# Optimization experiments

Hardware: AMD Instinct MI355X
Metric: run time of the kernel (lower is better)

The kernel has to match this reference:

```python
import jax, jax.numpy as jnp
import numpy as np

B, N, S, C1, C2, CIN, CO = 16, 4096, 1024, 128, 256, 384, 128
BN_EPS = 1e-5


def _bn(x, g, b):
    # BatchNorm1d in training mode: biased batch stats over (B, L) per channel.
    m = x.mean(axis=(0, 1))
    v = x.var(axis=(0, 1))
    return (x - m) * jax.lax.rsqrt(v + BN_EPS) * g + b


def _gelu(x):
    return jax.nn.gelu(x, approximate=False)  # torch nn.GELU default (erf)


def _conv1x1(x, w, b):
    # x: (B, L, Cin), w: (Cout, Cin) -> (B, L, Cout)
    return jnp.einsum('blc,oc->blo', x, w) + b


def setup_inputs() -> dict:
    ks = jax.random.split(jax.random.key(0), 20)
    sc = 0.05
    return {
        'xyz1': jax.random.normal(ks[0], (B, N, 3), jnp.float32),
        'xyz2': jax.random.normal(ks[1], (B, S, 3), jnp.float32),
        'points1': jax.random.normal(ks[2], (B, N, C1), jnp.float32),
        'points2': jax.random.normal(ks[3], (B, S, C2), jnp.float32),
        'fuse_w': jax.random.normal(ks[4], (CO, CIN), jnp.float32) * sc,
        'fuse_b': jax.random.normal(ks[5], (CO,), jnp.float32) * sc,
        'fuse_g': jnp.ones((CO,), jnp.float32),
        'fuse_bt': jnp.zeros((CO,), jnp.float32),
        'w1': jax.random.normal(ks[6], (CO, CO), jnp.float32) * sc,
        'b1': jax.random.normal(ks[7], (CO,), jnp.float32) * sc,
        'g1': jnp.ones((CO,), jnp.float32),
        'bt1': jnp.zeros((CO,), jnp.float32),
        'w2': jax.random.normal(ks[8], (CO, CO), jnp.float32) * sc,
        'b2': jax.random.normal(ks[9], (CO,), jnp.float32) * sc,
        'g2': jnp.ones((CO,), jnp.float32),
        'bt2': jnp.zeros((CO,), jnp.float32),
    }


def reference(xyz1, xyz2, points1, points2,
              fuse_w, fuse_b, fuse_g, fuse_bt,
              w1, b1, g1, bt1, w2, b2, g2, bt2):
    # pairwise euclidean distances (B, N, S) without (B,N,S,3) intermediate
    sq = (jnp.sum(xyz1 * xyz1, -1)[:, :, None]
          + jnp.sum(xyz2 * xyz2, -1)[:, None, :]
          - 2.0 * jnp.einsum('bnd,bsd->bns', xyz1, xyz2))
    dists = jnp.sqrt(jnp.maximum(sq, 1e-12))
    # 3 nearest neighbors, ascending distance
    neg_d3, idx = jax.lax.top_k(-dists, 3)        # (B, N, 3)
    d3 = -neg_d3
    dist_recip = 1.0 / (d3 + 1e-8)
    weight = dist_recip / jnp.sum(dist_recip, axis=-1, keepdims=True)
    gathered = points2[jnp.arange(B)[:, None, None], idx]  # (B, N, 3, C2)
    interp = jnp.sum(gathered * weight[..., None], axis=2)  # (B, N, C2)

    new_points = jnp.concatenate([points1, interp], axis=-1)  # (B, N, CIN)
    x = _gelu(_bn(_conv1x1(new_points, fuse_w, fuse_b), fuse_g, fuse_bt))
    # ConvBNReLURes1D block (groups=1, res_expansion=1.0)
    h = _gelu(_bn(_conv1x1(x, w1, b1), g1, bt1))
    h = _bn(_conv1x1(h, w2, b2), g2, bt2)
    return _gelu(h + x)  # (B, N, CO)
```

## Files before the change

### kernel.cpp

```cpp
#include <hip/hip_runtime.h>
#include <hip/hip_bf16.h>
#include <math.h>

#define B_   16
#define N_   4096
#define S_   1024
#define C1_  128
#define C2_  256
#define CIN_ 384
#define CO_  128
#define ROWS (B_ * N_)

typedef __attribute__((ext_vector_type(8))) __bf16 bf16x8;
typedef __attribute__((ext_vector_type(8))) short  s16x8;
typedef __attribute__((ext_vector_type(4))) float  f32x4;

__device__ inline float bf2f(short s) {
  unsigned u = ((unsigned)(unsigned short)s) << 16;
  float f; __builtin_memcpy(&f, &u, 4); return f;
}
__device__ inline short f2bf(float f) {
  __hip_bfloat16 h = __float2bfloat16(f);
  short s; __builtin_memcpy(&s, &h, 2); return s;
}
__device__ inline float gelu_f(float v) {
  return 0.5f * v * (1.f + erff(v * 0.70710678118654752f));
}
__device__ inline f32x4 mfma_bf16(s16x8 a, s16x8 b, f32x4 c) {
  return __builtin_amdgcn_mfma_f32_16x16x32_bf16(
      __builtin_bit_cast(bf16x8, a), __builtin_bit_cast(bf16x8, b), c, 0, 0, 0);
}

__global__ __launch_bounds__(256) void prep_kernel(
    const float* __restrict__ fw, const float* __restrict__ w1,
    const float* __restrict__ w2, short* __restrict__ fwb,
    short* __restrict__ w1b, short* __restrict__ w2b, float* __restrict__ stats)
{
  int i = blockIdx.x * 256 + threadIdx.x;
  if (i < CO_ * CIN_) fwb[i] = f2bf(fw[i]);
  if (i < CO_ * CO_) { w1b[i] = f2bf(w1[i]); w2b[i] = f2bf(w2[i]); }
  if (i < 768) stats[i] = 0.f;
}

__global__ __launch_bounds__(256) void knn_kernel(
    const float* __restrict__ xyz1, const float* __restrict__ xyz2,
    int* __restrict__ idxs, float* __restrict__ wts)
{
  __shared__ float4 pts[S_];
  const int b = blockIdx.y;
  const float* p2 = xyz2 + (size_t)b * S_ * 3;
  for (int j = threadIdx.x; j < S_; j += 256) {
    float x = p2[j*3+0], y = p2[j*3+1], z = p2[j*3+2];
    pts[j] = make_float4(x, y, z, x*x + y*y + z*z);
  }
  __syncthreads();
  const int n = blockIdx.x * 256 + threadIdx.x;
  const float* q = xyz1 + ((size_t)b * N_ + n) * 3;
  const float qx = q[0], qy = q[1], qz = q[2];
  const float qq = qx*qx + qy*qy + qz*qz;
  float d0 = 3.4e38f, d1 = 3.4e38f, d2 = 3.4e38f;
  int   i0 = 0, i1 = 0, i2 = 0;
  #pragma unroll 4
  for (int j = 0; j < S_; ++j) {
    float4 p = pts[j];
    float d = qq + p.w - 2.f * (qx*p.x + qy*p.y + qz*p.z);
    bool c2 = d < d2;
    d2 = c2 ? d : d2;  i2 = c2 ? j : i2;
    bool c1 = d2 < d1;
    float td = d1; int ti = i1;
    d1 = c1 ? d2 : d1; i1 = c1 ? i2 : i1;
    d2 = c1 ? td : d2; i2 = c1 ? ti : i2;
    bool c0 = d1 < d0;
    td = d0; ti = i0;
    d0 = c0 ? d1 : d0; i0 = c0 ? i1 : i0;
    d1 = c0 ? td : d1; i1 = c0 ? ti : i1;
  }
  float r0 = 1.f / (sqrtf(fmaxf(d0, 1e-12f)) + 1e-8f);
  float r1 = 1.f / (sqrtf(fmaxf(d1, 1e-12f)) + 1e-8f);
  float r2 = 1.f / (sqrtf(fmaxf(d2, 1e-12f)) + 1e-8f);
  float rs = 1.f / (r0 + r1 + r2);
  size_t o = ((size_t)b * N_ + n) * 3;
  idxs[o+0] = i0; idxs[o+1] = i1; idxs[o+2] = i2;
  wts [o+0] = r0*rs; wts[o+1] = r1*rs; wts[o+2] = r2*rs;
}

__global__ __launch_bounds__(384) void interp_kernel(
    const float* __restrict__ points1, const float* __restrict__ points2,
    const int* __restrict__ idxs, const float* __restrict__ wts,
    short* __restrict__ np_out)
{
  const int rid = blockIdx.x;
  const int b = rid >> 12;
  const int t = threadIdx.x;
  short* out = np_out + (size_t)rid * CIN_;
  if (t < C1_) {
    out[t] = f2bf(points1[(size_t)rid * C1_ + t]);
  } else {
    const int c = t - C1_;
    const int* id = idxs + (size_t)rid * 3;
    const float* w = wts + (size_t)rid * 3;
    const float* p2 = points2 + (size_t)b * S_ * C2_;
    float v = w[0] * p2[(size_t)id[0] * C2_ + c]
            + w[1] * p2[(size_t)id[1] * C2_ + c]
            + w[2] * p2[(size_t)id[2] * C2_ + c];
    out[t] = f2bf(v);
  }
}

template<int K>
__global__ __launch_bounds__(256) void gemm_bn_kernel(
    const short* __restrict__ A, const short* __restrict__ W,
    short* __restrict__ Raw, float* __restrict__ gsum, float* __restrict__ gsq)
{
  const int tid  = threadIdx.x;
  const int wave = tid >> 6, lane = tid & 63;
  const int l16  = lane & 15, lk = lane >> 4;
  const int row0 = blockIdx.x * 128 + wave * 32;

  __shared__ float ssum[CO_], ssq[CO_];
  if (tid < CO_) { ssum[tid] = 0.f; ssq[tid] = 0.f; }

  f32x4 acc[2][8];
  #pragma unroll
  for (int m = 0; m < 2; ++m)
    #pragma unroll
    for (int n = 0; n < 8; ++n) acc[m][n] = f32x4{0.f, 0.f, 0.f, 0.f};

  const short* a0 = A + (size_t)(row0 + l16) * K + lk * 8;
  const short* a1 = a0 + (size_t)16 * K;
  const short* w0 = W + (size_t)l16 * K + lk * 8;

  #pragma unroll 4
  for (int kk = 0; kk < K; kk += 32) {
    s16x8 af0 = *(const s16x8*)(a0 + kk);
    s16x8 af1 = *(const s16x8*)(a1 + kk);
    s16x8 wf[8];
    #pragma unroll
    for (int n = 0; n < 8; ++n)
      wf[n] = *(const s16x8*)(w0 + (size_t)n * 16 * K + kk);
    #pragma unroll
    for (int n = 0; n < 8; ++n) {
      acc[0][n] = mfma_bf16(af0, wf[n], acc[0][n]);
      acc[1][n] = mfma_bf16(af1, wf[n], acc[1][n]);
    }
  }
  __syncthreads();

  #pragma unroll
  for (int n = 0; n < 8; ++n) {
    float s = 0.f, q = 0.f;
    #pragma unroll
    for (int m = 0; m < 2; ++m)
      #pragma unroll
      for (int r = 0; r < 4; ++r) { float v = acc[m][n][r]; s += v; q += v*v; }
    s += __shfl_xor(s, 16); q += __shfl_xor(q, 16);
    s += __shfl_xor(s, 32); q += __shfl_xor(q, 32);
    if (lane < 16) {
      atomicAdd(&ssum[n*16 + l16], s);
      atomicAdd(&ssq [n*16 + l16], q);
    }
  }

  #pragma unroll
  for (int m = 0; m < 2; ++m)
    #pragma unroll
    for (int n = 0; n < 8; ++n)
      #pragma unroll
      for (int r = 0; r < 4; ++r) {
        int row = row0 + m*16 + lk*4 + r;
        Raw[(size_t)row * CO_ + n*16 + l16] = f2bf(acc[m][n][r]);
      }

  __syncthreads();
  if (tid < CO_)      atomicAdd(&gsum[tid],        ssum[tid]);
  else                atomicAdd(&gsq [tid - CO_],  ssq [tid - CO_]);
}

template<bool FINAL>
__global__ __launch_bounds__(256) void bn_act_kernel(
    const short* __restrict__ raw, const float* __restrict__ gsum,
    const float* __restrict__ gsq, const float* __restrict__ gamma,
    const float* __restrict__ beta, const short* __restrict__ xres,
    void* __restrict__ outp)
{
  __shared__ float ssc[CO_], ssh[CO_];
  const int tid = threadIdx.x;
  if (tid < CO_) {
    const float inv = 1.f / (float)ROWS;
    float mean = gsum[tid] * inv;
    float var  = gsq[tid] * inv - mean * mean;
    float sc   = gamma[tid] * rsqrtf(var + 1e-5f);
    ssc[tid] = sc;
    ssh[tid] = beta[tid] - mean * sc;
  }
  __syncthreads();
  const int gid = blockIdx.x * 256 + tid;
  float sc[8], sh[8];
  const int cpos = (gid & 15) * 8;
  #pragma unroll
  for (int j = 0; j < 8; ++j) { sc[j] = ssc[cpos + j]; sh[j] = ssh[cpos + j]; }
  const int NCHUNK = ROWS * CO_ / 8;
  const int stride = gridDim.x * 256;
  for (int ch = gid; ch < NCHUNK; ch += stride) {
    s16x8 rv = ((const s16x8*)raw)[ch];
    if (!FINAL) {
      s16x8 ov;
      #pragma unroll
      for (int j = 0; j < 8; ++j)
        ov[j] = f2bf(gelu_f(bf2f(rv[j]) * sc[j] + sh[j]));
      ((s16x8*)outp)[ch] = ov;
    } else {
      s16x8 xv = ((const s16x8*)xres)[ch];
      f32x4 o0, o1;
      #pragma unroll
      for (int j = 0; j < 4; ++j)
        o0[j] = gelu_f(bf2f(rv[j]) * sc[j] + sh[j] + bf2f(xv[j]));
      #pragma unroll
      for (int j = 0; j < 4; ++j)
        o1[j] = gelu_f(bf2f(rv[j+4]) * sc[j+4] + sh[j+4] + bf2f(xv[j+4]));
      ((f32x4*)outp)[2*(size_t)ch]     = o0;
      ((f32x4*)outp)[2*(size_t)ch + 1] = o1;
    }
  }
}

extern "C" void kernel_launch(void* const* d_in, const int* in_sizes, int n_in,
                              void* d_out, int out_size, void* d_ws, size_t ws_size,
                              hipStream_t stream) {
  const float* xyz1    = (const float*)d_in[0];
  const float* xyz2    = (const float*)d_in[1];
  const float* points1 = (const float*)d_in[2];
  const float* points2 = (const float*)d_in[3];
  const float* fuse_w  = (const float*)d_in[4];
  const float* fuse_g  = (const float*)d_in[6];
  const float* fuse_bt = (const float*)d_in[7];
  const float* w1      = (const float*)d_in[8];
  const float* g1      = (const float*)d_in[10];
  const float* bt1     = (const float*)d_in[11];
  const float* w2      = (const float*)d_in[12];
  const float* g2      = (const float*)d_in[14];
  const float* bt2     = (const float*)d_in[15];

  char* ws = (char*)d_ws;
  short* np_b  = (short*)(ws);
  short* x_b   = (short*)(ws);
  short* h_b   = (short*)(ws + 16777216);
  short* raw   = (short*)(ws + 50331648);
  short* wf_b  = (short*)(ws + 67108864);
  short* w1_b  = (short*)(ws + 67207168);
  short* w2_b  = (short*)(ws + 67239936);
  int*   idxs  = (int*)  (ws + 67272704);
  float* wts   = (float*)(ws + 68059136);
  float* stats = (float*)(ws + 68845568);
  float *sum1 = stats,       *sq1 = stats + 128;
  float *sum2 = stats + 256, *sq2 = stats + 384;
  float *sum3 = stats + 512, *sq3 = stats + 640;

  prep_kernel<<<192, 256, 0, stream>>>(fuse_w, w1, w2, wf_b, w1_b, w2_b, stats);
  knn_kernel<<<dim3(N_/256, B_), 256, 0, stream>>>(xyz1, xyz2, idxs, wts);
  interp_kernel<<<ROWS, 384, 0, stream>>>(points1, points2, idxs, wts, np_b);

  gemm_bn_kernel<CIN_><<<ROWS/128, 256, 0, stream>>>(np_b, wf_b, raw, sum1, sq1);
  bn_act_kernel<false><<<2048, 256, 0, stream>>>(raw, sum1, sq1, fuse_g, fuse_bt, nullptr, x_b);

  gemm_bn_kernel<CO_><<<ROWS/128, 256, 0, stream>>>(x_b, w1_b, raw, sum2, sq2);
  bn_act_kernel<false><<<2048, 256, 0, stream>>>(raw, sum2, sq2, g1, bt1, nullptr, h_b);

  gemm_bn_kernel<CO_><<<ROWS/128, 256, 0, stream>>>(h_b, w2_b, raw, sum3, sq3);
  bn_act_kernel<true><<<2048, 256, 0, stream>>>(raw, sum3, sq3, g2, bt2, x_b, d_out);
}
```

Before: 358.6 us.

## Fuse interpolation into first GEMM, split KNN across 8 lanes per query

Removes the separate interp kernel and its bf16 intermediate by gathering and weighting points2 rows and converting points1 directly inside the first GEMM's K loop. The KNN kernel now assigns 8 threads per query, each scanning a strided subset of candidates, then merges partial top-3 lists with xor shuffles; it also drops qq from the inner loop and adds it back at the end. The GEMM is transposed so weights are the A operand, and the epilogue writes 4-wide bf16 vectors with a shuffle-based stats reduction. The fused GEMM now performs scattered fp32 gathers inside its inner loop, which may stall the MFMA pipeline.

```diff
diff --git a/kernel.cpp b/kernel.cpp
--- a/kernel.cpp
+++ b/kernel.cpp
@@ -13,6 +13,7 @@
 
 typedef __attribute__((ext_vector_type(8))) __bf16 bf16x8;
 typedef __attribute__((ext_vector_type(8))) short  s16x8;
+typedef __attribute__((ext_vector_type(4))) short  s16x4;
 typedef __attribute__((ext_vector_type(4))) float  f32x4;
 
 __device__ inline float bf2f(short s) {
@@ -29,6 +30,12 @@
 __device__ inline f32x4 mfma_bf16(s16x8 a, s16x8 b, f32x4 c) {
   return __builtin_amdgcn_mfma_f32_16x16x32_bf16(
       __builtin_bit_cast(bf16x8, a), __builtin_bit_cast(bf16x8, b), c, 0, 0, 0);
+}
+__device__ inline s16x8 pack8(f32x4 a, f32x4 b) {
+  s16x8 r;
+  #pragma unroll
+  for (int j = 0; j < 4; ++j) { r[j] = f2bf(a[j]); r[j+4] = f2bf(b[j]); }
+  return r;
 }
 
 __global__ __launch_bounds__(256) void prep_kernel(
@@ -48,63 +55,154 @@
 {
   __shared__ float4 pts[S_];
   const int b = blockIdx.y;
-  const float* p2 = xyz2 + (size_t)b * S_ * 3;
+  const float* pp = xyz2 + (size_t)b * S_ * 3;
   for (int j = threadIdx.x; j < S_; j += 256) {
-    float x = p2[j*3+0], y = p2[j*3+1], z = p2[j*3+2];
+    float x = pp[j*3+0], y = pp[j*3+1], z = pp[j*3+2];
     pts[j] = make_float4(x, y, z, x*x + y*y + z*z);
   }
   __syncthreads();
-  const int n = blockIdx.x * 256 + threadIdx.x;
+  const int t   = blockIdx.x * 256 + threadIdx.x;
+  const int n   = t >> 3;
+  const int sub = t & 7;
   const float* q = xyz1 + ((size_t)b * N_ + n) * 3;
   const float qx = q[0], qy = q[1], qz = q[2];
   const float qq = qx*qx + qy*qy + qz*qz;
+
   float d0 = 3.4e38f, d1 = 3.4e38f, d2 = 3.4e38f;
   int   i0 = 0, i1 = 0, i2 = 0;
-  #pragma unroll 4
-  for (int j = 0; j < S_; ++j) {
-    float4 p = pts[j];
-    float d = qq + p.w - 2.f * (qx*p.x + qy*p.y + qz*p.z);
-    bool c2 = d < d2;
-    d2 = c2 ? d : d2;  i2 = c2 ? j : i2;
-    bool c1 = d2 < d1;
-    float td = d1; int ti = i1;
+  auto ins = [&](float d, int i) {
+    bool c2 = d < d2;  d2 = c2 ? d : d2;  i2 = c2 ? i : i2;
+    bool c1 = d2 < d1; float td = d1; int ti = i1;
     d1 = c1 ? d2 : d1; i1 = c1 ? i2 : i1;
     d2 = c1 ? td : d2; i2 = c1 ? ti : i2;
-    bool c0 = d1 < d0;
-    td = d0; ti = i0;
+    bool c0 = d1 < d0; td = d0; ti = i0;
     d0 = c0 ? d1 : d0; i0 = c0 ? i1 : i0;
     d1 = c0 ? td : d1; i1 = c0 ? ti : i1;
-  }
-  float r0 = 1.f / (sqrtf(fmaxf(d0, 1e-12f)) + 1e-8f);
-  float r1 = 1.f / (sqrtf(fmaxf(d1, 1e-12f)) + 1e-8f);
-  float r2 = 1.f / (sqrtf(fmaxf(d2, 1e-12f)) + 1e-8f);
-  float rs = 1.f / (r0 + r1 + r2);
-  size_t o = ((size_t)b * N_ + n) * 3;
-  idxs[o+0] = i0; idxs[o+1] = i1; idxs[o+2] = i2;
-  wts [o+0] = r0*rs; wts[o+1] = r1*rs; wts[o+2] = r2*rs;
-}
-
-__global__ __launch_bounds__(384) void interp_kernel(
-    const float* __restrict__ points1, const float* __restrict__ points2,
+  };
+  #pragma unroll 4
+  for (int it = 0; it < S_ / 8; ++it) {
+    int j = it * 8 + sub;
+    float4 p = pts[j];
+    float dot = fmaf(qz, p.z, fmaf(qy, p.y, qx * p.x));
+    float d = fmaf(-2.f, dot, p.w);
+    ins(d, j);
+  }
+  #pragma unroll
+  for (int delta = 1; delta < 8; delta <<= 1) {
+    float e0 = __shfl_xor(d0, delta), e1 = __shfl_xor(d1, delta), e2 = __shfl_xor(d2, delta);
+    int   j0 = __shfl_xor(i0, delta), j1 = __shfl_xor(i1, delta), j2 = __shfl_xor(i2, delta);
+    ins(e0, j0); ins(e1, j1); ins(e2, j2);
+  }
+  if (sub == 0) {
+    float r0 = 1.f / (sqrtf(fmaxf(d0 + qq, 1e-12f)) + 1e-8f);
+    float r1 = 1.f / (sqrtf(fmaxf(d1 + qq, 1e-12f)) + 1e-8f);
+    float r2 = 1.f / (sqrtf(fmaxf(d2 + qq, 1e-12f)) + 1e-8f);
+    float rs = 1.f / (r0 + r1 + r2);
+    size_t o = ((size_t)b * N_ + n) * 3;
+    idxs[o+0] = i0; idxs[o+1] = i1; idxs[o+2] = i2;
+    wts [o+0] = r0*rs; wts[o+1] = r1*rs; wts[o+2] = r2*rs;
+  }
+}
+
+__device__ inline void epilogue_store_stats(
+    f32x4 (&acc)[8][2], int row0, int l16, int lk,
+    short* __restrict__ Raw, float* __restrict__ ssum, float* __restrict__ ssq)
+{
+  #pragma unroll
+  for (int m = 0; m < 8; ++m) {
+    f32x4 sv = acc[m][0] + acc[m][1];
+    f32x4 qv = acc[m][0]*acc[m][0] + acc[m][1]*acc[m][1];
+    #pragma unroll
+    for (int r = 0; r < 4; ++r) {
+      float s = sv[r], q = qv[r];
+      s += __shfl_xor(s, 1); q += __shfl_xor(q, 1);
+      s += __shfl_xor(s, 2); q += __shfl_xor(q, 2);
+      s += __shfl_xor(s, 4); q += __shfl_xor(q, 4);
+      s += __shfl_xor(s, 8); q += __shfl_xor(q, 8);
+      if (l16 == 0) {
+        int c = m*16 + lk*4 + r;
+        atomicAdd(&ssum[c], s); atomicAdd(&ssq[c], q);
+      }
+    }
+    #pragma unroll
+    for (int nf = 0; nf < 2; ++nf) {
+      s16x4 pv;
+      #pragma unroll
+      for (int r = 0; r < 4; ++r) pv[r] = f2bf(acc[m][nf][r]);
+      *(s16x4*)(Raw + (size_t)(row0 + nf*16 + l16) * CO_ + m*16 + lk*4) = pv;
+    }
+  }
+}
+
+__global__ __launch_bounds__(256) void gemm1_fused_kernel(
+    const float* __restrict__ p1, const float* __restrict__ p2,
     const int* __restrict__ idxs, const float* __restrict__ wts,
-    short* __restrict__ np_out)
-{
-  const int rid = blockIdx.x;
-  const int b = rid >> 12;
-  const int t = threadIdx.x;
-  short* out = np_out + (size_t)rid * CIN_;
-  if (t < C1_) {
-    out[t] = f2bf(points1[(size_t)rid * C1_ + t]);
-  } else {
-    const int c = t - C1_;
-    const int* id = idxs + (size_t)rid * 3;
-    const float* w = wts + (size_t)rid * 3;
-    const float* p2 = points2 + (size_t)b * S_ * C2_;
-    float v = w[0] * p2[(size_t)id[0] * C2_ + c]
-            + w[1] * p2[(size_t)id[1] * C2_ + c]
-            + w[2] * p2[(size_t)id[2] * C2_ + c];
-    out[t] = f2bf(v);
-  }
+    const short* __restrict__ W, short* __restrict__ Raw,
+    float* __restrict__ gsum, float* __restrict__ gsq)
+{
+  const int tid  = threadIdx.x;
+  const int wave = tid >> 6, lane = tid & 63;
+  const int l16  = lane & 15, lk = lane >> 4;
+  const int row0 = blockIdx.x * 128 + wave * 32;
+
+  __shared__ float ssum[CO_], ssq[CO_];
+  if (tid < CO_) { ssum[tid] = 0.f; ssq[tid] = 0.f; }
+
+  const int r0 = row0 + l16, r1 = r0 + 16;
+  const int bb = row0 >> 12;
+  const float* p2b = p2 + (size_t)bb * S_ * C2_;
+  const float* ga0 = p2b + (size_t)idxs[(size_t)r0*3+0] * C2_;
+  const float* ga1 = p2b + (size_t)idxs[(size_t)r0*3+1] * C2_;
+  const float* ga2 = p2b + (size_t)idxs[(size_t)r0*3+2] * C2_;
+  const float  wa0 = wts[(size_t)r0*3+0], wa1 = wts[(size_t)r0*3+1], wa2 = wts[(size_t)r0*3+2];
+  const float* gb0 = p2b + (size_t)idxs[(size_t)r1*3+0] * C2_;
+  const float* gb1 = p2b + (size_t)idxs[(size_t)r1*3+1] * C2_;
+  const float* gb2 = p2b + (size_t)idxs[(size_t)r1*3+2] * C2_;
+  const float  wb0 = wts[(size_t)r1*3+0], wb1 = wts[(size_t)r1*3+1], wb2 = wts[(size_t)r1*3+2];
+
+  f32x4 acc[8][2];
+  #pragma unroll
+  for (int m = 0; m < 8; ++m)
+    #pragma unroll
+    for (int nf = 0; nf < 2; ++nf) acc[m][nf] = f32x4{0.f,0.f,0.f,0.f};
+
+  const short* wbase = W + (size_t)l16 * CIN_ + lk * 8;
+  const float* p1r0  = p1 + (size_t)r0 * C1_ + lk * 8;
+  const float* p1r1  = p1 + (size_t)r1 * C1_ + lk * 8;
+
+  #pragma unroll
+  for (int kk = 0; kk < 128; kk += 32) {
+    s16x8 bf0 = pack8(*(const f32x4*)(p1r0 + kk), *(const f32x4*)(p1r0 + kk + 4));
+    s16x8 bf1 = pack8(*(const f32x4*)(p1r1 + kk), *(const f32x4*)(p1r1 + kk + 4));
+    #pragma unroll
+    for (int m = 0; m < 8; ++m) {
+      s16x8 wf = *(const s16x8*)(wbase + (size_t)m*16*CIN_ + kk);
+      acc[m][0] = mfma_bf16(wf, bf0, acc[m][0]);
+      acc[m][1] = mfma_bf16(wf, bf1, acc[m][1]);
+    }
+  }
+  #pragma unroll 4
+  for (int kk2 = 0; kk2 < 256; kk2 += 32) {
+    const int c = kk2 + lk * 8;
+    f32x4 v0a = wa0 * *(const f32x4*)(ga0 + c)     + wa1 * *(const f32x4*)(ga1 + c)     + wa2 * *(const f32x4*)(ga2 + c);
+    f32x4 v0b = wa0 * *(const f32x4*)(ga0 + c + 4) + wa1 * *(const f32x4*)(ga1 + c + 4) + wa2 * *(const f32x4*)(ga2 + c + 4);
+    f32x4 v1a = wb0 * *(const f32x4*)(gb0 + c)     + wb1 * *(const f32x4*)(gb1 + c)     + wb2 * *(const f32x4*)(gb2 + c);
+    f32x4 v1b = wb0 * *(const f32x4*)(gb0 + c + 4) + wb1 * *(const f32x4*)(gb1 + c + 4) + wb2 * *(const f32x4*)(gb2 + c + 4);
+    s16x8 bf0 = pack8(v0a, v0b);
+    s16x8 bf1 = pack8(v1a, v1b);
+    #pragma unroll
+    for (int m = 0; m < 8; ++m) {
+      s16x8 wf = *(const s16x8*)(wbase + (size_t)m*16*CIN_ + 128 + kk2);
+      acc[m][0] = mfma_bf16(wf, bf0, acc[m][0]);
+      acc[m][1] = mfma_bf16(wf, bf1, acc[m][1]);
+    }
+  }
+
+  __syncthreads();
+  epilogue_store_stats(acc, row0, l16, lk, Raw, ssum, ssq);
+  __syncthreads();
+  if (tid < CO_)      atomicAdd(&gsum[tid],       ssum[tid]);
+  else                atomicAdd(&gsq[tid - CO_],  ssq[tid - CO_]);
 }
 
 template<int K>
@@ -120,60 +218,33 @@
   __shared__ float ssum[CO_], ssq[CO_];
   if (tid < CO_) { ssum[tid] = 0.f; ssq[tid] = 0.f; }
 
-  f32x4 acc[2][8];
-  #pragma unroll
-  for (int m = 0; m < 2; ++m)
-    #pragma unroll
-    for (int n = 0; n < 8; ++n) acc[m][n] = f32x4{0.f, 0.f, 0.f, 0.f};
-
-  const short* a0 = A + (size_t)(row0 + l16) * K + lk * 8;
-  const short* a1 = a0 + (size_t)16 * K;
-  const short* w0 = W + (size_t)l16 * K + lk * 8;
+  f32x4 acc[8][2];
+  #pragma unroll
+  for (int m = 0; m < 8; ++m)
+    #pragma unroll
+    for (int nf = 0; nf < 2; ++nf) acc[m][nf] = f32x4{0.f,0.f,0.f,0.f};
+
+  const short* a0    = A + (size_t)(row0 + l16) * K + lk * 8;
+  const short* a1    = a0 + (size_t)16 * K;
+  const short* wbase = W + (size_t)l16 * K + lk * 8;
 
   #pragma unroll 4
   for (int kk = 0; kk < K; kk += 32) {
-    s16x8 af0 = *(const s16x8*)(a0 + kk);
-    s16x8 af1 = *(const s16x8*)(a1 + kk);
-    s16x8 wf[8];
-    #pragma unroll
-    for (int n = 0; n < 8; ++n)
-      wf[n] = *(const s16x8*)(w0 + (size_t)n * 16 * K + kk);
-    #pragma unroll
-    for (int n = 0; n < 8; ++n) {
-      acc[0][n] = mfma_bf16(af0, wf[n], acc[0][n]);
-      acc[1][n] = mfma_bf16(af1, wf[n], acc[1][n]);
-    }
-  }
-  __syncthreads();
-
-  #pragma unroll
-  for (int n = 0; n < 8; ++n) {
-    float s = 0.f, q = 0.f;
-    #pragma unroll
-    for (int m = 0; m < 2; ++m)
-      #pragma unroll
-      for (int r = 0; r < 4; ++r) { float v = acc[m][n][r]; s += v; q += v*v; }
-    s += __shfl_xor(s, 16); q += __shfl_xor(q, 16);
-    s += __shfl_xor(s, 32); q += __shfl_xor(q, 32);
-    if (lane < 16) {
-      atomicAdd(&ssum[n*16 + l16], s);
-      atomicAdd(&ssq [n*16 + l16], q);
-    }
-  }
-
-  #pragma unroll
-  for (int m = 0; m < 2; ++m)
-    #pragma unroll
-    for (int n = 0; n < 8; ++n)
-      #pragma unroll
-      for (int r = 0; r < 4; ++r) {
-        int row = row0 + m*16 + lk*4 + r;
-        Raw[(size_t)row * CO_ + n*16 + l16] = f2bf(acc[m][n][r]);
-      }
-
-  __syncthreads();
-  if (tid < CO_)      atomicAdd(&gsum[tid],        ssum[tid]);
-  else                atomicAdd(&gsq [tid - CO_],  ssq [tid - CO_]);
+    s16x8 bf0 = *(const s16x8*)(a0 + kk);
+    s16x8 bf1 = *(const s16x8*)(a1 + kk);
+    #pragma unroll
+    for (int m = 0; m < 8; ++m) {
+      s16x8 wf = *(const s16x8*)(wbase + (size_t)m*16*K + kk);
+      acc[m][0] = mfma_bf16(wf, bf0, acc[m][0]);
+      acc[m][1] = mfma_bf16(wf, bf1, acc[m][1]);
+    }
+  }
+
+  __syncthreads();
+  epilogue_store_stats(acc, row0, l16, lk, Raw, ssum, ssq);
+  __syncthreads();
+  if (tid < CO_)      atomicAdd(&gsum[tid],       ssum[tid]);
+  else                atomicAdd(&gsq[tid - CO_],  ssq[tid - CO_]);
 }
 
 template<bool FINAL>
@@ -242,25 +313,24 @@
   const float* bt2     = (const float*)d_in[15];
 
   char* ws = (char*)d_ws;
-  short* np_b  = (short*)(ws);
   short* x_b   = (short*)(ws);
   short* h_b   = (short*)(ws + 16777216);
-  short* raw   = (short*)(ws + 50331648);
-  short* wf_b  = (short*)(ws + 67108864);
-  short* w1_b  = (short*)(ws + 67207168);
-  short* w2_b  = (short*)(ws + 67239936);
-  int*   idxs  = (int*)  (ws + 67272704);
-  float* wts   = (float*)(ws + 68059136);
-  float* stats = (float*)(ws + 68845568);
+  short* raw   = (short*)(ws + 33554432);
+  short* wf_b  = (short*)(ws + 50331648);
+  short* w1_b  = (short*)(ws + 50429952);
+  short* w2_b  = (short*)(ws + 50462720);
+  int*   idxs  = (int*)  (ws + 50495488);
+  float* wts   = (float*)(ws + 51281920);
+  float* stats = (float*)(ws + 52068352);
   float *sum1 = stats,       *sq1 = stats + 128;
   float *sum2 = stats + 256, *sq2 = stats + 384;
   float *sum3 = stats + 512, *sq3 = stats + 640;
 
   prep_kernel<<<192, 256, 0, stream>>>(fuse_w, w1, w2, wf_b, w1_b, w2_b, stats);
-  knn_kernel<<<dim3(N_/256, B_), 256, 0, stream>>>(xyz1, xyz2, idxs, wts);
-  interp_kernel<<<ROWS, 384, 0, stream>>>(points1, points2, idxs, wts, np_b);
-
-  gemm_bn_kernel<CIN_><<<ROWS/128, 256, 0, stream>>>(np_b, wf_b, raw, sum1, sq1);
+  knn_kernel<<<dim3(N_*8/256, B_), 256, 0, stream>>>(xyz1, xyz2, idxs, wts);
+
+  gemm1_fused_kernel<<<ROWS/128, 256, 0, stream>>>(points1, points2, idxs, wts,
+                                                   wf_b, raw, sum1, sq1);
   bn_act_kernel<false><<<2048, 256, 0, stream>>>(raw, sum1, sq1, fuse_g, fuse_bt, nullptr, x_b);
 
   gemm_bn_kernel<CO_><<<ROWS/128, 256, 0, stream>>>(x_b, w1_b, raw, sum2, sq2);
```

Result: faster. 311.5 us (-13.1%).
